# Performance work log

Hardware: AMD Instinct MI355X
Metric: run time of the kernel (lower is better)

Reference implementation:

```python
import jax, jax.numpy as jnp
import numpy as np
import math

B, NQ, NK = 32, 1024, 1024
DQ = DK = DV = 512
H = 8
EPS = 1e-5


def _layernorm(x, g, b):
    mu = jnp.mean(x, axis=-1, keepdims=True)
    var = jnp.mean(jnp.square(x - mu), axis=-1, keepdims=True)
    return (x - mu) * jax.lax.rsqrt(var + EPS) * g + b


def setup_inputs() -> dict:
    key = jax.random.key(0)
    ks = jax.random.split(key, 8)
    s = 0.03  # small init scale for linear weights
    return {
        "Q": jax.random.normal(ks[0], (B, NQ, DQ), jnp.float32),
        "K": jax.random.normal(ks[1], (B, NK, DK), jnp.float32),
        "Wq": jax.random.normal(ks[2], (DQ, DV), jnp.float32) * s,
        "bq": jnp.zeros((DV,), jnp.float32),
        "Wk": jax.random.normal(ks[3], (DK, DV), jnp.float32) * s,
        "bk": jnp.zeros((DV,), jnp.float32),
        "Wv": jax.random.normal(ks[4], (DK, DV), jnp.float32) * s,
        "bv": jnp.zeros((DV,), jnp.float32),
        "Wo": jax.random.normal(ks[5], (DV, DV), jnp.float32) * s,
        "bo": jnp.zeros((DV,), jnp.float32),
        "g0": jnp.ones((DV,), jnp.float32),
        "beta0": jnp.zeros((DV,), jnp.float32),
        "g1": jnp.ones((DV,), jnp.float32),
        "beta1": jnp.zeros((DV,), jnp.float32),
    }


def reference(Q, K, Wq, bq, Wk, bk, Wv, bv, Wo, bo, g0, beta0, g1, beta1):
    b, nq, _ = Q.shape
    nk = K.shape[1]
    d = DV // H  # head dim (dim_split)

    q = Q @ Wq + bq            # [B, Nq, DV]
    k = K @ Wk + bk            # [B, Nk, DV]
    v = K @ Wv + bv            # [B, Nk, DV]

    # torch.cat(x.split(d, 2), 0) == reshape to [B,N,H,d] then stack heads on batch dim
    qh = q.reshape(b, nq, H, d).transpose(2, 0, 1, 3)  # [H, B, Nq, d]
    kh = k.reshape(b, nk, H, d).transpose(2, 0, 1, 3)  # [H, B, Nk, d]
    vh = v.reshape(b, nk, H, d).transpose(2, 0, 1, 3)  # [H, B, Nk, d]

    # NOTE: scaled by sqrt(dim_V), and softmax over the QUERY axis (torch dim=1)
    scores = jnp.einsum('hbqd,hbkd->hbqk', qh, kh) / math.sqrt(DV)
    A = jax.nn.softmax(scores, axis=2)                 # over Nq (faithful to source)
    oh = qh + jnp.einsum('hbqk,hbkd->hbqd', A, vh)     # residual on Q_

    out = oh.transpose(1, 2, 0, 3).reshape(b, nq, DV)  # merge heads back
    out = _layernorm(out, g0, beta0)
    out = out + jax.nn.relu(out @ Wo + bo)
    out = _layernorm(out, g1, beta1)
    return out
```

## Files before the change

kernel.cpp:

```cpp
#include <hip/hip_runtime.h>

#define Bz  32
#define NQz 1024
#define NKz 1024
#define SCALE 0.04419417382415922f

typedef __bf16 bf16_t;
typedef bf16_t bf16x8 __attribute__((ext_vector_type(8)));
typedef bf16_t bf16x4 __attribute__((ext_vector_type(4)));
typedef float  f32x4  __attribute__((ext_vector_type(4)));

#define MFMA16(a, b, c) __builtin_amdgcn_mfma_f32_16x16x32_bf16(a, b, c, 0, 0, 0)

#define SBAR() asm volatile("s_barrier" ::: "memory")
#define WAITVM(n) asm volatile("s_waitcnt vmcnt(" #n ")" ::: "memory")
#define WAITVL(n) asm volatile("s_waitcnt vmcnt(" #n ") lgkmcnt(0)" ::: "memory")

__device__ __forceinline__ void gll16(const void* g, void* l) {
  __builtin_amdgcn_global_load_lds(
      (const __attribute__((address_space(1))) void*)g,
      (__attribute__((address_space(3))) void*)l, 16, 0, 0);
}

__device__ __forceinline__ float fexp2(float x) {
#if __has_builtin(__builtin_amdgcn_exp2f)
  return __builtin_amdgcn_exp2f(x);
#else
  float r;
  asm("v_exp_f32 %0, %1" : "=v"(r) : "v"(x));
  return r;
#endif
}

__device__ __forceinline__ bf16x8 cvt8(float4 a, float4 b) {
  bf16x8 r;
  r[0] = (bf16_t)a.x; r[1] = (bf16_t)a.y; r[2] = (bf16_t)a.z; r[3] = (bf16_t)a.w;
  r[4] = (bf16_t)b.x; r[5] = (bf16_t)b.y; r[6] = (bf16_t)b.z; r[7] = (bf16_t)b.w;
  return r;
}

__global__ void transpose_w(const float* __restrict__ W0, const float* __restrict__ W1,
                            const float* __restrict__ W2, const float* __restrict__ W3,
                            bf16_t* __restrict__ out) {
  __shared__ float tile[32][33];
  const float* W = blockIdx.z == 0 ? W0 : blockIdx.z == 1 ? W1 : blockIdx.z == 2 ? W2 : W3;
  bf16_t* o = out + (size_t)blockIdx.z * 512 * 512;
  const int n0 = blockIdx.x * 32, k0 = blockIdx.y * 32;
  const int tx = threadIdx.x, ty = threadIdx.y;
  for (int i = 0; i < 4; i++)
    tile[ty + i * 8][tx] = W[(size_t)(k0 + ty + i * 8) * 512 + n0 + tx];
  __syncthreads();
  for (int i = 0; i < 4; i++)
    o[(size_t)(n0 + ty + i * 8) * 512 + k0 + tx] = (bf16_t)tile[tx][ty + i * 8];
}

template <int DUAL>
__global__ __launch_bounds__(256) void gemm_f32a(const float* __restrict__ A,
                                                 const bf16_t* __restrict__ Wt,
                                                 const float* __restrict__ b0v,
                                                 const float* __restrict__ b1v,
                                                 float mult0,
                                                 bf16_t* __restrict__ C0,
                                                 bf16_t* __restrict__ C1) {
  __shared__ __align__(16) bf16_t As[128][40];
  __shared__ __align__(16) bf16_t Bs[2][128 * 32];
  const int t = threadIdx.x;
  const int wave = t >> 6, lane = t & 63;
  const int quad = lane >> 4, l16 = lane & 15;
  const int wm = wave & 1, wn = wave >> 1;
  const int m0 = blockIdx.x * 128, n0 = blockIdx.y * 128;
  const int r = t >> 1, half = t & 1;
  const int drow = lane >> 2;
  const int dg = (lane & 3) ^ ((lane >> 3) & 3);

  f32x4 acc[4][4] = {};

  const float* arow = A + (size_t)(m0 + r) * 512 + half * 16;
  const bf16_t* wrow = Wt + (size_t)(n0 + wave * 16 + drow) * 512 + dg * 8;

  for (int p = 0; p < 2; p++)
    gll16(wrow + (size_t)(p * 64) * 512, &Bs[0][(p * 256 + wave * 64) * 8]);
  float4 a0 = *(const float4*)(arow + 0);
  float4 a1 = *(const float4*)(arow + 4);
  float4 a2 = *(const float4*)(arow + 8);
  float4 a3 = *(const float4*)(arow + 12);

  for (int it = 0; it < 16; it++) {
    const int cur = it & 1;
    if (it < 15)
      for (int p = 0; p < 2; p++)
        gll16(wrow + (it + 1) * 32 + (size_t)(p * 64) * 512,
              &Bs[cur ^ 1][(p * 256 + wave * 64) * 8]);
    *(bf16x8*)&As[r][half * 16 + 0] = cvt8(a0, a1);
    *(bf16x8*)&As[r][half * 16 + 8] = cvt8(a2, a3);
    if (it < 15) {
      const float* ap = arow + (it + 1) * 32;
      a0 = *(const float4*)(ap + 0);
      a1 = *(const float4*)(ap + 4);
      a2 = *(const float4*)(ap + 8);
      a3 = *(const float4*)(ap + 12);
      WAITVL(6);
    } else {
      WAITVL(0);
    }
    SBAR();
    bf16x8 af[4], bfv[4];
    for (int mt = 0; mt < 4; mt++)
      af[mt] = *(const bf16x8*)&As[wm * 64 + mt * 16 + l16][quad * 8];
    for (int nt = 0; nt < 4; nt++) {
      const int rB = wn * 64 + nt * 16 + l16;
      bfv[nt] = *(const bf16x8*)&Bs[cur][rB * 32 + ((quad ^ ((rB >> 1) & 3)) * 8)];
    }
    for (int mt = 0; mt < 4; mt++)
      for (int nt = 0; nt < 4; nt++)
        acc[mt][nt] = MFMA16(af[mt], bfv[nt], acc[mt][nt]);
    SBAR();
  }

  const float* bias = (!DUAL || n0 < 512) ? b0v : b1v;
  bf16_t* C = (!DUAL || n0 < 512) ? C0 : C1;
  const float mult = (!DUAL || n0 < 512) ? mult0 : 1.0f;
  const int nb = (!DUAL || n0 < 512) ? n0 : n0 - 512;
  for (int mt = 0; mt < 4; mt++) {
    for (int nt = 0; nt < 4; nt++) {
      const int row = m0 + wm * 64 + mt * 16 + quad * 4;
      const int col = nb + wn * 64 + nt * 16 + l16;
      const float bv = bias[col];
      for (int rg = 0; rg < 4; rg++)
        C[(size_t)(row + rg) * 512 + col] = (bf16_t)((acc[mt][nt][rg] + bv) * mult);
    }
  }
}

__global__ __launch_bounds__(256) void gemm_bf16a(const bf16_t* __restrict__ A,
                                                  const bf16_t* __restrict__ Wt,
                                                  const float* __restrict__ bias,
                                                  bf16_t* __restrict__ C) {
  __shared__ __align__(16) bf16_t As[128][40];
  __shared__ __align__(16) bf16_t Bs[2][128 * 32];
  const int t = threadIdx.x;
  const int wave = t >> 6, lane = t & 63;
  const int quad = lane >> 4, l16 = lane & 15;
  const int wm = wave & 1, wn = wave >> 1;
  const int m0 = blockIdx.x * 128, n0 = blockIdx.y * 128;
  const int r = t >> 1, half = t & 1;
  const int drow = lane >> 2;
  const int dg = (lane & 3) ^ ((lane >> 3) & 3);

  f32x4 acc[4][4] = {};

  const bf16_t* arow = A + (size_t)(m0 + r) * 512 + half * 16;
  const bf16_t* wrow = Wt + (size_t)(n0 + wave * 16 + drow) * 512 + dg * 8;

  for (int p = 0; p < 2; p++)
    gll16(wrow + (size_t)(p * 64) * 512, &Bs[0][(p * 256 + wave * 64) * 8]);
  bf16x8 v0 = *(const bf16x8*)(arow + 0);
  bf16x8 v1 = *(const bf16x8*)(arow + 8);

  for (int it = 0; it < 16; it++) {
    const int cur = it & 1;
    if (it < 15)
      for (int p = 0; p < 2; p++)
        gll16(wrow + (it + 1) * 32 + (size_t)(p * 64) * 512,
              &Bs[cur ^ 1][(p * 256 + wave * 64) * 8]);
    *(bf16x8*)&As[r][half * 16 + 0] = v0;
    *(bf16x8*)&As[r][half * 16 + 8] = v1;
    if (it < 15) {
      const bf16_t* ap = arow + (it + 1) * 32;
      v0 = *(const bf16x8*)(ap + 0);
      v1 = *(const bf16x8*)(ap + 8);
      WAITVL(4);
    } else {
      WAITVL(0);
    }
    SBAR();
    bf16x8 af[4], bfv[4];
    for (int mt = 0; mt < 4; mt++)
      af[mt] = *(const bf16x8*)&As[wm * 64 + mt * 16 + l16][quad * 8];
    for (int nt = 0; nt < 4; nt++) {
      const int rB = wn * 64 + nt * 16 + l16;
      bfv[nt] = *(const bf16x8*)&Bs[cur][rB * 32 + ((quad ^ ((rB >> 1) & 3)) * 8)];
    }
    for (int mt = 0; mt < 4; mt++)
      for (int nt = 0; nt < 4; nt++)
        acc[mt][nt] = MFMA16(af[mt], bfv[nt], acc[mt][nt]);
    SBAR();
  }

  for (int mt = 0; mt < 4; mt++) {
    for (int nt = 0; nt < 4; nt++) {
      const int row = m0 + wm * 64 + mt * 16 + quad * 4;
      const int col = n0 + wn * 64 + nt * 16 + l16;
      const float bv = bias[col];
      for (int rg = 0; rg < 4; rg++) {
        float v = acc[mt][nt][rg] + bv;
        float x = (float)A[(size_t)(row + rg) * 512 + col];
        C[(size_t)(row + rg) * 512 + col] = (bf16_t)(x + fmaxf(v, 0.f));
      }
    }
  }
}

__global__ __launch_bounds__(256) void attn_stats(const bf16_t* __restrict__ qp,
                                                  const bf16_t* __restrict__ kp,
                                                  const bf16_t* __restrict__ vp,
                                                  bf16_t* __restrict__ Vt) {
  __shared__ __align__(16) bf16_t Vs[128][72];
  __shared__ __align__(16) bf16_t Qs[2][64 * 64];
  __shared__ float ls[128];
  const int t = threadIdx.x;
  const int wave = t >> 6, lane = t & 63;
  const int quad = lane >> 4, l16 = lane & 15;
  const int id = blockIdx.x;
  const int kb = ((id >> 3) & 7) * 128;
  const int hb = (id & 7) * 32 + (id >> 6);
  const int h = hb >> 5, b = hb & 31;
  const bf16_t* qbase = qp + (size_t)b * NQz * 512 + h * 64;
  const bf16_t* kbase = kp + (size_t)b * NKz * 512 + h * 64;
  const int drow = lane >> 3;
  const int dg = (lane & 7) ^ drow;

  {
    const int r = t >> 1, half = t & 1;
    const bf16_t* vr = vp + (size_t)b * NKz * 512 + (size_t)(kb + r) * 512 + h * 64 + half * 32;
    *(bf16x8*)&Vs[r][half * 32 + 0]  = *(const bf16x8*)(vr + 0);
    *(bf16x8*)&Vs[r][half * 32 + 8]  = *(const bf16x8*)(vr + 8);
    *(bf16x8*)&Vs[r][half * 32 + 16] = *(const bf16x8*)(vr + 16);
    *(bf16x8*)&Vs[r][half * 32 + 24] = *(const bf16x8*)(vr + 24);
  }

  bf16x8 aK[2][2];
  for (int mt = 0; mt < 2; mt++) {
    const bf16_t* kr = kbase + (size_t)(kb + wave * 32 + mt * 16 + l16) * 512 + quad * 8;
    aK[mt][0] = *(const bf16x8*)kr;
    aK[mt][1] = *(const bf16x8*)(kr + 32);
  }

  for (int p = 0; p < 2; p++) {
    const bf16_t* src = qbase + (size_t)(p * 32 + wave * 8 + drow) * 512 + dg * 8;
    gll16(src, &Qs[0][(p * 256 + wave * 64) * 8]);
  }

  f32x4 lacc[2] = {};
  for (int it = 0; it < 16; it++) {
    const int cur = it & 1;
    if (it < 15) {
      const int qn = (it + 1) * 64;
      for (int p = 0; p < 2; p++) {
        const bf16_t* src = qbase + (size_t)(qn + p * 32 + wave * 8 + drow) * 512 + dg * 8;
        gll16(src, &Qs[cur ^ 1][(p * 256 + wave * 64) * 8]);
      }
      WAITVM(2);
    } else {
      WAITVM(0);
    }
    SBAR();
    for (int nt = 0; nt < 4; nt++) {
      const int rQ = nt * 16 + l16;
      bf16x8 b0 = *(const bf16x8*)&Qs[cur][rQ * 64 + ((quad ^ (rQ & 7)) * 8)];
      bf16x8 b1 = *(const bf16x8*)&Qs[cur][rQ * 64 + (((quad + 4) ^ (rQ & 7)) * 8)];
      for (int mt = 0; mt < 2; mt++) {
        f32x4 s = {0.f, 0.f, 0.f, 0.f};
        s = MFMA16(aK[mt][0], b0, s);
        s = MFMA16(aK[mt][1], b1, s);
        lacc[mt][0] += fexp2(s[0]);
        lacc[mt][1] += fexp2(s[1]);
        lacc[mt][2] += fexp2(s[2]);
        lacc[mt][3] += fexp2(s[3]);
      }
    }
    SBAR();
  }
  for (int mt = 0; mt < 2; mt++) {
    for (int rg = 0; rg < 4; rg++) {
      float v = lacc[mt][rg];
      v += __shfl_xor(v, 1);
      v += __shfl_xor(v, 2);
      v += __shfl_xor(v, 4);
      v += __shfl_xor(v, 8);
      if (l16 == 0) ls[wave * 32 + mt * 16 + quad * 4 + rg] = 1.0f / v;
    }
  }
  __syncthreads();
  const int d = t >> 2, kc = (t & 3) * 32;
  bf16_t* vtr = Vt + (size_t)hb * 64 * 1024 + (size_t)d * 1024 + kb + kc;
  for (int c = 0; c < 4; c++) {
    bf16x8 o;
    for (int j = 0; j < 8; j++)
      o[j] = (bf16_t)((float)Vs[kc + c * 8 + j][d] * ls[kc + c * 8 + j]);
    *(bf16x8*)(vtr + c * 8) = o;
  }
}

__global__ __launch_bounds__(256) void attn_out(const bf16_t* __restrict__ qp,
                                                const bf16_t* __restrict__ kp,
                                                const bf16_t* __restrict__ Vt,
                                                bf16_t* __restrict__ oh) {
  __shared__ __align__(16) bf16_t Ks[2][64 * 64];
  __shared__ __align__(16) bf16_t Vts[2][64 * 64];
  __shared__ __align__(16) bf16_t Ps[128][72];
  const int t = threadIdx.x;
  const int wave = t >> 6, lane = t & 63;
  const int quad = lane >> 4, l16 = lane & 15;
  const int id = blockIdx.x;
  const int qt = (id >> 3) & 7;
  const int hb = (id & 7) * 32 + (id >> 6);
  const int h = hb >> 5, b = hb & 31;
  const int q0 = qt * 128;
  const bf16_t* qbase = qp + (size_t)b * NQz * 512 + h * 64;
  const bf16_t* kbase = kp + (size_t)b * NKz * 512 + h * 64;
  const bf16_t* vtbase = Vt + (size_t)hb * 64 * 1024;
  const int drow = lane >> 3;
  const int dg = (lane & 7) ^ drow;

  bf16x8 bQ[2][2];
  for (int nt = 0; nt < 2; nt++) {
    const bf16_t* qr = qbase + (size_t)(q0 + wave * 32 + nt * 16 + l16) * 512 + quad * 8;
    bQ[nt][0] = *(const bf16x8*)qr;
    bQ[nt][1] = *(const bf16x8*)(qr + 32);
  }

  for (int p = 0; p < 2; p++) {
    const bf16_t* ksrc = kbase + (size_t)(p * 32 + wave * 8 + drow) * 512 + dg * 8;
    gll16(ksrc, &Ks[0][(p * 256 + wave * 64) * 8]);
    const bf16_t* vsrc = vtbase + (size_t)(p * 32 + wave * 8 + drow) * 1024 + dg * 8;
    gll16(vsrc, &Vts[0][(p * 256 + wave * 64) * 8]);
  }

  f32x4 acc[2][4] = {};
  for (int it = 0; it < 16; it++) {
    const int kk = it * 64;
    const int cur = it & 1;
    if (it < 15) {
      const int kn = kk + 64;
      for (int p = 0; p < 2; p++) {
        const bf16_t* ksrc = kbase + (size_t)(kn + p * 32 + wave * 8 + drow) * 512 + dg * 8;
        gll16(ksrc, &Ks[cur ^ 1][(p * 256 + wave * 64) * 8]);
        const bf16_t* vsrc = vtbase + (size_t)(p * 32 + wave * 8 + drow) * 1024 + kn + dg * 8;
        gll16(vsrc, &Vts[cur ^ 1][(p * 256 + wave * 64) * 8]);
      }
      WAITVM(4);
    } else {
      WAITVM(0);
    }
    SBAR();
    for (int mt = 0; mt < 4; mt++) {
      const int rK = mt * 16 + l16;
      bf16x8 a0 = *(const bf16x8*)&Ks[cur][rK * 64 + ((quad ^ (rK & 7)) * 8)];
      bf16x8 a1 = *(const bf16x8*)&Ks[cur][rK * 64 + (((quad + 4) ^ (rK & 7)) * 8)];
      for (int nt = 0; nt < 2; nt++) {
        f32x4 s = {0.f, 0.f, 0.f, 0.f};
        s = MFMA16(a0, bQ[nt][0], s);
        s = MFMA16(a1, bQ[nt][1], s);
        bf16x4 pk;
        pk[0] = (bf16_t)fexp2(s[0]);
        pk[1] = (bf16_t)fexp2(s[1]);
        pk[2] = (bf16_t)fexp2(s[2]);
        pk[3] = (bf16_t)fexp2(s[3]);
        *(bf16x4*)&Ps[wave * 32 + nt * 16 + l16][mt * 16 + quad * 4] = pk;
      }
    }
    bf16x8 aP[2][2];
    for (int mt = 0; mt < 2; mt++) {
      aP[mt][0] = *(const bf16x8*)&Ps[wave * 32 + mt * 16 + l16][quad * 8];
      aP[mt][1] = *(const bf16x8*)&Ps[wave * 32 + mt * 16 + l16][quad * 8 + 32];
    }
    for (int nd = 0; nd < 4; nd++) {
      const int rV = nd * 16 + l16;
      bf16x8 b0 = *(const bf16x8*)&Vts[cur][rV * 64 + ((quad ^ (rV & 7)) * 8)];
      bf16x8 b1 = *(const bf16x8*)&Vts[cur][rV * 64 + (((quad + 4) ^ (rV & 7)) * 8)];
      for (int mt = 0; mt < 2; mt++) {
        acc[mt][nd] = MFMA16(aP[mt][0], b0, acc[mt][nd]);
        acc[mt][nd] = MFMA16(aP[mt][1], b1, acc[mt][nd]);
      }
    }
    SBAR();
  }
  for (int mt = 0; mt < 2; mt++)
    for (int nd = 0; nd < 4; nd++)
      for (int rg = 0; rg < 4; rg++)
        Ps[wave * 32 + mt * 16 + quad * 4 + rg][nd * 16 + l16] = (bf16_t)acc[mt][nd][rg];
  const int row = wave * 32 + (lane >> 1), cc = (lane & 1) * 32;
  bf16_t* orow = oh + ((size_t)b * NQz + q0 + row) * 512 + h * 64 + cc;
  for (int c = 0; c < 4; c++)
    *(bf16x8*)(orow + c * 8) = *(const bf16x8*)&Ps[row][cc + c * 8];
}

template <int RES, int F32OUT>
__global__ __launch_bounds__(256) void ln_k(const bf16_t* __restrict__ x,
                                            const bf16_t* __restrict__ res,
                                            const float* __restrict__ g,
                                            const float* __restrict__ be,
                                            bf16_t* __restrict__ yb,
                                            float* __restrict__ yf) {
  const int wave = threadIdx.x >> 6, lane = threadIdx.x & 63;
  const size_t row = (size_t)blockIdx.x * 4 + wave;
  bf16x8 xv = *(const bf16x8*)(x + row * 512 + lane * 8);
  float xf[8];
  for (int i = 0; i < 8; i++) xf[i] = (float)xv[i];
  if (RES) {
    bf16x8 rv = *(const bf16x8*)(res + row * 512 + lane * 8);
    for (int i = 0; i < 8; i++) xf[i] += (float)rv[i];
  }
  float s = 0.f, sq = 0.f;
  for (int i = 0; i < 8; i++) { s += xf[i]; sq += xf[i] * xf[i]; }
  for (int off = 1; off < 64; off <<= 1) {
    s += __shfl_xor(s, off);
    sq += __shfl_xor(sq, off);
  }
  const float mu = s * (1.0f / 512.0f);
  const float var = sq * (1.0f / 512.0f) - mu * mu;
  const float rstd = rsqrtf(var + 1e-5f);
  float4 gv0 = *(const float4*)(g + lane * 8);
  float4 gv1 = *(const float4*)(g + lane * 8 + 4);
  float4 bv0 = *(const float4*)(be + lane * 8);
  float4 bv1 = *(const float4*)(be + lane * 8 + 4);
  float gg[8] = {gv0.x, gv0.y, gv0.z, gv0.w, gv1.x, gv1.y, gv1.z, gv1.w};
  float bb[8] = {bv0.x, bv0.y, bv0.z, bv0.w, bv1.x, bv1.y, bv1.z, bv1.w};
  float o[8];
  for (int i = 0; i < 8; i++) o[i] = (xf[i] - mu) * rstd * gg[i] + bb[i];
  if (F32OUT) {
    float4 o0 = {o[0], o[1], o[2], o[3]}, o1 = {o[4], o[5], o[6], o[7]};
    *(float4*)(yf + row * 512 + lane * 8) = o0;
    *(float4*)(yf + row * 512 + lane * 8 + 4) = o1;
  } else {
    bf16x8 ov;
    for (int i = 0; i < 8; i++) ov[i] = (bf16_t)o[i];
    *(bf16x8*)(yb + row * 512 + lane * 8) = ov;
  }
}

extern "C" void kernel_launch(void* const* d_in, const int* in_sizes, int n_in,
                              void* d_out, int out_size, void* d_ws, size_t ws_size,
                              hipStream_t stream) {
  (void)in_sizes; (void)n_in; (void)out_size; (void)ws_size;
  const float* Q   = (const float*)d_in[0];
  const float* K   = (const float*)d_in[1];
  const float* Wq  = (const float*)d_in[2];
  const float* bq  = (const float*)d_in[3];
  const float* Wk  = (const float*)d_in[4];
  const float* bk  = (const float*)d_in[5];
  const float* Wv  = (const float*)d_in[6];
  const float* bv  = (const float*)d_in[7];
  const float* Wo  = (const float*)d_in[8];
  const float* bo  = (const float*)d_in[9];
  const float* g0  = (const float*)d_in[10];
  const float* be0 = (const float*)d_in[11];
  const float* g1  = (const float*)d_in[12];
  const float* be1 = (const float*)d_in[13];
  float* outp = (float*)d_out;

  char* w = (char*)d_ws;
  bf16_t* Wt  = (bf16_t*)w;
  bf16_t* qp  = (bf16_t*)(w + (2ull << 20));
  bf16_t* kp  = (bf16_t*)(w + (34ull << 20));
  bf16_t* vp  = (bf16_t*)(w + (66ull << 20));
  bf16_t* Vt  = (bf16_t*)(w + (98ull << 20));
  bf16_t* ohb = (bf16_t*)(w + (130ull << 20));
  bf16_t* x0b = vp;
  bf16_t* oh2 = kp;

  transpose_w<<<dim3(16, 16, 4), dim3(32, 8), 0, stream>>>(Wq, Wk, Wv, Wo, Wt);
  gemm_f32a<0><<<dim3(256, 4), 256, 0, stream>>>(Q, Wt, bq, nullptr, 1.0f, qp, nullptr);
  gemm_f32a<1><<<dim3(256, 8), 256, 0, stream>>>(K, Wt + (1 << 18), bk, bv,
                                                 SCALE * 1.4426950408889634f, kp, vp);
  attn_stats<<<2048, 256, 0, stream>>>(qp, kp, vp, Vt);
  attn_out<<<2048, 256, 0, stream>>>(qp, kp, Vt, ohb);
  ln_k<1, 0><<<8192, 256, 0, stream>>>(ohb, qp, g0, be0, x0b, nullptr);
  gemm_bf16a<<<dim3(256, 4), 256, 0, stream>>>(x0b, Wt + 3 * (1 << 18), bo, oh2);
  ln_k<0, 1><<<8192, 256, 0, stream>>>(oh2, nullptr, g1, be1, nullptr, outp);
}
```

Baseline: 492.1 us.

## Load V fragments directly to registers, add MFMA priority, remap GEMM tile order

```diff
diff --git a/kernel.cpp b/kernel.cpp
--- a/kernel.cpp
+++ b/kernel.cpp
@@ -68,7 +68,9 @@
   const int wave = t >> 6, lane = t & 63;
   const int quad = lane >> 4, l16 = lane & 15;
   const int wm = wave & 1, wn = wave >> 1;
-  const int m0 = blockIdx.x * 128, n0 = blockIdx.y * 128;
+  const int flat = blockIdx.y * gridDim.x + blockIdx.x;
+  const int m0 = (DUAL ? (flat >> 3) : (flat >> 2)) * 128;
+  const int n0 = (DUAL ? (flat & 7) : (flat & 3)) * 128;
   const int r = t >> 1, half = t & 1;
   const int drow = lane >> 2;
   const int dg = (lane & 3) ^ ((lane >> 3) & 3);
@@ -142,7 +144,8 @@
   const int wave = t >> 6, lane = t & 63;
   const int quad = lane >> 4, l16 = lane & 15;
   const int wm = wave & 1, wn = wave >> 1;
-  const int m0 = blockIdx.x * 128, n0 = blockIdx.y * 128;
+  const int flat = blockIdx.y * gridDim.x + blockIdx.x;
+  const int m0 = (flat >> 2) * 128, n0 = (flat & 3) * 128;
   const int r = t >> 1, half = t & 1;
   const int drow = lane >> 2;
   const int dg = (lane & 3) ^ ((lane >> 3) & 3);
@@ -261,8 +264,10 @@
       bf16x8 b1 = *(const bf16x8*)&Qs[cur][rQ * 64 + (((quad + 4) ^ (rQ & 7)) * 8)];
       for (int mt = 0; mt < 2; mt++) {
         f32x4 s = {0.f, 0.f, 0.f, 0.f};
+        __builtin_amdgcn_s_setprio(1);
         s = MFMA16(aK[mt][0], b0, s);
         s = MFMA16(aK[mt][1], b1, s);
+        __builtin_amdgcn_s_setprio(0);
         lacc[mt][0] += fexp2(s[0]);
         lacc[mt][1] += fexp2(s[1]);
         lacc[mt][2] += fexp2(s[2]);
@@ -292,12 +297,11 @@
   }
 }
 
-__global__ __launch_bounds__(256) void attn_out(const bf16_t* __restrict__ qp,
-                                                const bf16_t* __restrict__ kp,
-                                                const bf16_t* __restrict__ Vt,
-                                                bf16_t* __restrict__ oh) {
+__global__ __launch_bounds__(256, 4) void attn_out(const bf16_t* __restrict__ qp,
+                                                   const bf16_t* __restrict__ kp,
+                                                   const bf16_t* __restrict__ Vt,
+                                                   bf16_t* __restrict__ oh) {
   __shared__ __align__(16) bf16_t Ks[2][64 * 64];
-  __shared__ __align__(16) bf16_t Vts[2][64 * 64];
   __shared__ __align__(16) bf16_t Ps[128][72];
   const int t = threadIdx.x;
   const int wave = t >> 6, lane = t & 63;
@@ -319,29 +323,34 @@
     bQ[nt][0] = *(const bf16x8*)qr;
     bQ[nt][1] = *(const bf16x8*)(qr + 32);
   }
+  const bf16_t* vrow[4];
+  for (int nd = 0; nd < 4; nd++)
+    vrow[nd] = vtbase + (size_t)(nd * 16 + l16) * 1024 + quad * 8;
 
   for (int p = 0; p < 2; p++) {
     const bf16_t* ksrc = kbase + (size_t)(p * 32 + wave * 8 + drow) * 512 + dg * 8;
     gll16(ksrc, &Ks[0][(p * 256 + wave * 64) * 8]);
-    const bf16_t* vsrc = vtbase + (size_t)(p * 32 + wave * 8 + drow) * 1024 + dg * 8;
-    gll16(vsrc, &Vts[0][(p * 256 + wave * 64) * 8]);
   }
 
   f32x4 acc[2][4] = {};
   for (int it = 0; it < 16; it++) {
     const int kk = it * 64;
     const int cur = it & 1;
+    bf16x8 vf[4][2];
+    for (int nd = 0; nd < 4; nd++) {
+      vf[nd][0] = *(const bf16x8*)(vrow[nd] + kk);
+      vf[nd][1] = *(const bf16x8*)(vrow[nd] + kk + 32);
+    }
+    __builtin_amdgcn_sched_barrier(0);
     if (it < 15) {
       const int kn = kk + 64;
       for (int p = 0; p < 2; p++) {
         const bf16_t* ksrc = kbase + (size_t)(kn + p * 32 + wave * 8 + drow) * 512 + dg * 8;
         gll16(ksrc, &Ks[cur ^ 1][(p * 256 + wave * 64) * 8]);
-        const bf16_t* vsrc = vtbase + (size_t)(p * 32 + wave * 8 + drow) * 1024 + kn + dg * 8;
-        gll16(vsrc, &Vts[cur ^ 1][(p * 256 + wave * 64) * 8]);
-      }
-      WAITVM(4);
+      }
+      WAITVM(10);
     } else {
-      WAITVM(0);
+      WAITVM(8);
     }
     SBAR();
     for (int mt = 0; mt < 4; mt++) {
@@ -350,8 +359,10 @@
       bf16x8 a1 = *(const bf16x8*)&Ks[cur][rK * 64 + (((quad + 4) ^ (rK & 7)) * 8)];
       for (int nt = 0; nt < 2; nt++) {
         f32x4 s = {0.f, 0.f, 0.f, 0.f};
+        __builtin_amdgcn_s_setprio(1);
         s = MFMA16(a0, bQ[nt][0], s);
         s = MFMA16(a1, bQ[nt][1], s);
+        __builtin_amdgcn_s_setprio(0);
         bf16x4 pk;
         pk[0] = (bf16_t)fexp2(s[0]);
         pk[1] = (bf16_t)fexp2(s[1]);
@@ -365,15 +376,14 @@
       aP[mt][0] = *(const bf16x8*)&Ps[wave * 32 + mt * 16 + l16][quad * 8];
       aP[mt][1] = *(const bf16x8*)&Ps[wave * 32 + mt * 16 + l16][quad * 8 + 32];
     }
+    __builtin_amdgcn_s_setprio(1);
     for (int nd = 0; nd < 4; nd++) {
-      const int rV = nd * 16 + l16;
-      bf16x8 b0 = *(const bf16x8*)&Vts[cur][rV * 64 + ((quad ^ (rV & 7)) * 8)];
-      bf16x8 b1 = *(const bf16x8*)&Vts[cur][rV * 64 + (((quad + 4) ^ (rV & 7)) * 8)];
       for (int mt = 0; mt < 2; mt++) {
-        acc[mt][nd] = MFMA16(aP[mt][0], b0, acc[mt][nd]);
-        acc[mt][nd] = MFMA16(aP[mt][1], b1, acc[mt][nd]);
-      }
-    }
+        acc[mt][nd] = MFMA16(aP[mt][0], vf[nd][0], acc[mt][nd]);
+        acc[mt][nd] = MFMA16(aP[mt][1], vf[nd][1], acc[mt][nd]);
+      }
+    }
+    __builtin_amdgcn_s_setprio(0);
     SBAR();
   }
   for (int mt = 0; mt < 2; mt++)
```

Result: slower. 580.1 us (+17.9%).
